# Kernel tuning notes

Hardware: AMD Instinct MI355X
Metric: run time of the kernel (lower is better)

## Reference

```python
import jax, jax.numpy as jnp
import numpy as np

B, L, H = 4, 2048, 1024
NH = 16
DK = H // NH


def setup_inputs() -> dict:
    key = jax.random.key(0)
    ks = jax.random.split(key, 9)
    s = 1.0 / np.sqrt(H)
    return {
        "x": jax.random.normal(ks[0], (B, L, H), dtype=jnp.float32),
        "Wq": jax.random.uniform(ks[1], (H, H), jnp.float32, -s, s),
        "bq": jnp.zeros((H,), jnp.float32),
        "Wk": jax.random.uniform(ks[2], (H, H), jnp.float32, -s, s),
        "bk": jnp.zeros((H,), jnp.float32),
        "Wv": jax.random.uniform(ks[3], (H, H), jnp.float32, -s, s),
        "bv": jnp.zeros((H,), jnp.float32),
        "Wo": jax.random.uniform(ks[4], (H, H), jnp.float32, -s, s),
        "bo": jnp.zeros((H,), jnp.float32),
    }


def reference(x, Wq, bq, Wk, bk, Wv, bv, Wo, bo):
    # Linear projections (torch Linear: x @ W.T + b), split heads -> (B, NH, L, DK)
    def proj(W, b):
        y = jnp.einsum("blh,oh->blo", x, W) + b
        return y.reshape(B, L, NH, DK).transpose(0, 2, 1, 3)

    q = proj(Wq, bq)
    k = proj(Wk, bk)
    v = proj(Wv, bv)

    scale = jnp.sqrt(jnp.asarray(DK, x.dtype))
    scores = jnp.einsum("bnqd,bnkd->bnqk", q, k) / scale  # (B, NH, L, L)
    attn = jax.nn.softmax(scores, axis=-1)
    # dropout is identity in eval mode
    context = jnp.einsum("bnqk,bnkd->bnqd", attn, v)
    context = context.transpose(0, 2, 1, 3).reshape(B, L, H)
    out = jnp.einsum("blh,oh->blo", context, Wo) + bo

    pooled = out.mean(axis=1)                 # (B, H)
    weights = attn.mean(axis=1).mean(axis=1)  # (B, L)
    return pooled, weights
```

## Files before the change

### kernel.cpp

```cpp
#include <hip/hip_runtime.h>
#include <math.h>

#define B_  4
#define L_  2048
#define H_  1024
#define NH_ 16
#define DK_ 64

#define QSC 0.18033688011112043f

typedef unsigned short ushort_t;
typedef __attribute__((ext_vector_type(8))) short short8;
typedef __attribute__((ext_vector_type(4))) float f32x4;

__device__ __forceinline__ ushort_t f2b(float f) {
    unsigned int u = __float_as_uint(f);
    return (ushort_t)((u + 0x7FFFu + ((u >> 16) & 1u)) >> 16);
}
__device__ __forceinline__ float b2f(ushort_t h) {
    return __uint_as_float(((unsigned int)h) << 16);
}
__device__ __forceinline__ float fexp2(float x) {
    return __builtin_amdgcn_exp2f(x);
}

__device__ __forceinline__ void gload_lds16(const void* g, void* l) {
    __builtin_amdgcn_global_load_lds((const __attribute__((address_space(1))) void*)g,
                                     (__attribute__((address_space(3))) void*)l, 16, 0, 0);
}

__device__ __forceinline__ void split8(const float4& a, const float4& b,
                                       short8& h, short8& l) {
    float f[8] = {a.x, a.y, a.z, a.w, b.x, b.y, b.z, b.w};
    #pragma unroll
    for (int e = 0; e < 8; ++e) {
        unsigned int u  = __float_as_uint(f[e]);
        float fh = __uint_as_float(u & 0xFFFF0000u);
        float r  = f[e] - fh;
        h[e] = (short)(u >> 16);
        l[e] = (short)(__float_as_uint(r) >> 16);
    }
}

__global__ __launch_bounds__(256) void wsplit_kernel(const float* __restrict__ src,
                                                     ushort_t* __restrict__ ph,
                                                     ushort_t* __restrict__ pl, int n4)
{
    int i = blockIdx.x * 256 + threadIdx.x;
    if (i < n4) {
        float4 v = ((const float4*)src)[i];
        ushort4 h, l;
        float f[4] = {v.x, v.y, v.z, v.w};
        ushort_t hh[4], ll[4];
        #pragma unroll
        for (int e = 0; e < 4; ++e) {
            hh[e] = f2b(f[e]);
            ll[e] = f2b(f[e] - b2f(hh[e]));
        }
        h.x = hh[0]; h.y = hh[1]; h.z = hh[2]; h.w = hh[3];
        l.x = ll[0]; l.y = ll[1]; l.z = ll[2]; l.w = ll[3];
        ((ushort4*)ph)[i] = h;
        ((ushort4*)pl)[i] = l;
    }
}

__global__ __launch_bounds__(256) void proj_split(
    const float* __restrict__ x,
    const ushort_t* __restrict__ Wqh, const ushort_t* __restrict__ Wql,
    const ushort_t* __restrict__ Wkh, const ushort_t* __restrict__ Wkl,
    const float* __restrict__ bq, const float* __restrict__ bk,
    ushort_t* __restrict__ qh, ushort_t* __restrict__ ql,
    ushort_t* __restrict__ kh, ushort_t* __restrict__ kl)
{
    const int z = blockIdx.z;
    const ushort_t* Wh = z ? Wkh : Wqh;
    const ushort_t* Wl = z ? Wkl : Wql;
    const float* bias  = z ? bk  : bq;
    ushort_t* dh       = z ? kh  : qh;
    ushort_t* dl       = z ? kl  : ql;
    const float qs     = z ? 1.0f : QSC;

    const int n0 = blockIdx.y * 128;
    const int o0 = blockIdx.x * 128;

    __shared__ float    Asf[128 * 32];
    __shared__ ushort_t Bsh[128 * 32];
    __shared__ ushort_t Bsl[128 * 32];

    const int t = threadIdx.x;
    const int lane = t & 63, w = t >> 6;
    const int ln = lane & 15, qd = lane >> 4;
    const int wy = w >> 1, wx = w & 1;

    int rxS[4], cxS[4];
    #pragma unroll
    for (int i = 0; i < 4; ++i) {
        int slot = i * 256 + t;
        rxS[i] = slot >> 3;
        cxS[i] = (slot & 7) ^ (rxS[i] & 7);
    }
    int rwS[2], cwS[2];
    #pragma unroll
    for (int i = 0; i < 2; ++i) {
        int slot = i * 256 + t;
        rwS[i] = slot >> 2;
        cwS[i] = (slot & 3) ^ ((rwS[i] >> 1) & 3);
    }

    f32x4 acc[4][4];
    #pragma unroll
    for (int i = 0; i < 4; ++i)
        #pragma unroll
        for (int j = 0; j < 4; ++j) acc[i][j] = (f32x4){0.f, 0.f, 0.f, 0.f};

    for (int k0 = 0; k0 < H_; k0 += 32) {
        __syncthreads();
        #pragma unroll
        for (int i = 0; i < 4; ++i)
            gload_lds16(x + (size_t)(n0 + rxS[i]) * H_ + k0 + cxS[i] * 4,
                        &Asf[i * 1024 + (t & ~63) * 4]);
        #pragma unroll
        for (int i = 0; i < 2; ++i) {
            gload_lds16(Wh + (size_t)(o0 + rwS[i]) * H_ + k0 + cwS[i] * 8,
                        &Bsh[i * 2048 + (t & ~63) * 8]);
            gload_lds16(Wl + (size_t)(o0 + rwS[i]) * H_ + k0 + cwS[i] * 8,
                        &Bsl[i * 2048 + (t & ~63) * 8]);
        }
        __syncthreads();

        short8 bh4[4], bl4[4];
        #pragma unroll
        for (int nt = 0; nt < 4; ++nt) {
            int row = wx * 64 + nt * 16 + ln;
            int sz = (qd ^ ((row >> 1) & 3)) << 3;
            bh4[nt] = *(const short8*)&Bsh[row * 32 + sz];
            bl4[nt] = *(const short8*)&Bsl[row * 32 + sz];
        }
        #pragma unroll
        for (int mt = 0; mt < 4; ++mt) {
            int row = wy * 64 + mt * 16 + ln;
            int r7 = row & 7;
            float4 fa = *(const float4*)&Asf[row * 32 + (((2 * qd)     ^ r7) << 2)];
            float4 fb = *(const float4*)&Asf[row * 32 + (((2 * qd + 1) ^ r7) << 2)];
            short8 ah, al;
            split8(fa, fb, ah, al);
            #pragma unroll
            for (int nt = 0; nt < 4; ++nt) {
                acc[mt][nt] = __builtin_amdgcn_mfma_f32_16x16x32_bf16(al, bh4[nt], acc[mt][nt], 0, 0, 0);
                acc[mt][nt] = __builtin_amdgcn_mfma_f32_16x16x32_bf16(ah, bl4[nt], acc[mt][nt], 0, 0, 0);
                acc[mt][nt] = __builtin_amdgcn_mfma_f32_16x16x32_bf16(ah, bh4[nt], acc[mt][nt], 0, 0, 0);
            }
        }
    }

    #pragma unroll
    for (int nt = 0; nt < 4; ++nt) {
        int o = o0 + wx * 64 + nt * 16 + ln;
        float bvv = bias[o];
        int hh = o >> 6, d = o & 63;
        #pragma unroll
        for (int mt = 0; mt < 4; ++mt) {
            #pragma unroll
            for (int r = 0; r < 4; ++r) {
                int n = n0 + wy * 64 + mt * 16 + qd * 4 + r;
                int bb = n >> 11, l = n & (L_ - 1);
                float val = (acc[mt][nt][r] + bvv) * qs;
                ushort_t vh = f2b(val);
                ushort_t vl = f2b(val - b2f(vh));
                size_t idx = (((size_t)(bb * NH_ + hh) * L_ + l) << 6) + d;
                dh[idx] = vh;
                dl[idx] = vl;
            }
        }
    }
}

__global__ __launch_bounds__(256) void attn_split(
    const ushort_t* __restrict__ qh, const ushort_t* __restrict__ ql,
    const ushort_t* __restrict__ kh, const ushort_t* __restrict__ kl,
    float* __restrict__ cs)
{
    const int qt = blockIdx.x & 15;
    const int bh = blockIdx.x >> 4;

    const int t = threadIdx.x;
    const int lane = t & 63, w = t >> 6;
    const int ln = lane & 15, qd = lane >> 4;

    __shared__ ushort_t Ksh[64 * 64];
    __shared__ ushort_t Ksl[64 * 64];
    __shared__ float cs_all[4][64];

    const size_t headoff = (size_t)bh * L_ * DK_;
    const size_t qoff0 = headoff + ((size_t)(qt * 128 + w * 32 + ln)) * DK_;
    const size_t qoff1 = qoff0 + 16 * DK_;
    short8 aqh[2][2], aql[2][2];
    aqh[0][0] = *(const short8*)(qh + qoff0 + qd * 8);
    aqh[0][1] = *(const short8*)(qh + qoff0 + 32 + qd * 8);
    aqh[1][0] = *(const short8*)(qh + qoff1 + qd * 8);
    aqh[1][1] = *(const short8*)(qh + qoff1 + 32 + qd * 8);
    aql[0][0] = *(const short8*)(ql + qoff0 + qd * 8);
    aql[0][1] = *(const short8*)(ql + qoff0 + 32 + qd * 8);
    aql[1][0] = *(const short8*)(ql + qoff1 + qd * 8);
    aql[1][1] = *(const short8*)(ql + qoff1 + 32 + qd * 8);

    int rowS[2], cS[2];
    #pragma unroll
    for (int i = 0; i < 2; ++i) {
        int slot = i * 256 + t;
        rowS[i] = slot >> 3;
        cS[i] = (slot & 7) ^ (rowS[i] & 7);
    }

    float l_run[2][4] = {};

    for (int kt = 0; kt < 32; ++kt) {
        __syncthreads();
        #pragma unroll
        for (int i = 0; i < 2; ++i)
            gload_lds16(kh + headoff + ((size_t)(kt * 64 + rowS[i]) << 6) + cS[i] * 8,
                        &Ksh[i * 2048 + (t & ~63) * 8]);
        __syncthreads();

        #pragma unroll
        for (int nt = 0; nt < 4; ++nt) {
            int kr = nt * 16 + ln;
            int sz0 = ((qd     ^ (kr & 7)) << 3);
            int sz1 = (((qd + 4) ^ (kr & 7)) << 3);
            short8 b0h = *(const short8*)&Ksh[kr * 64 + sz0];
            short8 b1h = *(const short8*)&Ksh[kr * 64 + sz1];
            #pragma unroll
            for (int s = 0; s < 2; ++s) {
                f32x4 zz = (f32x4){0.f, 0.f, 0.f, 0.f};
                zz = __builtin_amdgcn_mfma_f32_16x16x32_bf16(aqh[s][0], b0h, zz, 0, 0, 0);
                zz = __builtin_amdgcn_mfma_f32_16x16x32_bf16(aqh[s][1], b1h, zz, 0, 0, 0);
                #pragma unroll
                for (int r = 0; r < 4; ++r)
                    l_run[s][r] += fexp2(zz[r]);
            }
        }
    }

    #pragma unroll
    for (int off = 1; off < 16; off <<= 1)
        #pragma unroll
        for (int s = 0; s < 2; ++s)
            #pragma unroll
            for (int r = 0; r < 4; ++r)
                l_run[s][r] += __shfl_xor(l_run[s][r], off);
    float inv_l[2][4];
    #pragma unroll
    for (int s = 0; s < 2; ++s)
        #pragma unroll
        for (int r = 0; r < 4; ++r) inv_l[s][r] = 1.0f / l_run[s][r];

    for (int kt = 0; kt < 32; ++kt) {
        __syncthreads();
        #pragma unroll
        for (int i = 0; i < 2; ++i) {
            gload_lds16(kh + headoff + ((size_t)(kt * 64 + rowS[i]) << 6) + cS[i] * 8,
                        &Ksh[i * 2048 + (t & ~63) * 8]);
            gload_lds16(kl + headoff + ((size_t)(kt * 64 + rowS[i]) << 6) + cS[i] * 8,
                        &Ksl[i * 2048 + (t & ~63) * 8]);
        }
        __syncthreads();

        float colp[4];
        #pragma unroll
        for (int nt = 0; nt < 4; ++nt) {
            int kr = nt * 16 + ln;
            int sz0 = ((qd     ^ (kr & 7)) << 3);
            int sz1 = (((qd + 4) ^ (kr & 7)) << 3);
            short8 b0h = *(const short8*)&Ksh[kr * 64 + sz0];
            short8 b1h = *(const short8*)&Ksh[kr * 64 + sz1];
            short8 b0l = *(const short8*)&Ksl[kr * 64 + sz0];
            short8 b1l = *(const short8*)&Ksl[kr * 64 + sz1];
            float cp = 0.f;
            #pragma unroll
            for (int s = 0; s < 2; ++s) {
                f32x4 zz = (f32x4){0.f, 0.f, 0.f, 0.f};
                zz = __builtin_amdgcn_mfma_f32_16x16x32_bf16(aql[s][0], b0h, zz, 0, 0, 0);
                zz = __builtin_amdgcn_mfma_f32_16x16x32_bf16(aql[s][1], b1h, zz, 0, 0, 0);
                zz = __builtin_amdgcn_mfma_f32_16x16x32_bf16(aqh[s][0], b0l, zz, 0, 0, 0);
                zz = __builtin_amdgcn_mfma_f32_16x16x32_bf16(aqh[s][1], b1l, zz, 0, 0, 0);
                zz = __builtin_amdgcn_mfma_f32_16x16x32_bf16(aqh[s][0], b0h, zz, 0, 0, 0);
                zz = __builtin_amdgcn_mfma_f32_16x16x32_bf16(aqh[s][1], b1h, zz, 0, 0, 0);
                cp += fexp2(zz[0]) * inv_l[s][0] + fexp2(zz[1]) * inv_l[s][1]
                    + fexp2(zz[2]) * inv_l[s][2] + fexp2(zz[3]) * inv_l[s][3];
            }
            colp[nt] = cp;
        }
        #pragma unroll
        for (int nt = 0; nt < 4; ++nt) {
            colp[nt] += __shfl_xor(colp[nt], 16);
            colp[nt] += __shfl_xor(colp[nt], 32);
        }
        float mine = (qd == 0) ? colp[0] : (qd == 1) ? colp[1] : (qd == 2) ? colp[2] : colp[3];
        cs_all[w][lane] = mine;
        __syncthreads();
        if (t < 64) {
            float tot = cs_all[0][t] + cs_all[1][t] + cs_all[2][t] + cs_all[3][t];
            atomicAdd(&cs[(size_t)bh * L_ + kt * 64 + t], tot);
        }
    }
}

__global__ __launch_bounds__(256) void ctx1_kernel(
    const float* __restrict__ cs, const float* __restrict__ x, float* __restrict__ T)
{
    const int o0 = blockIdx.x * 64, b = blockIdx.y, l0 = blockIdx.z * 256;
    const int t = threadIdx.x, o = t & 63, hg = t >> 6;
    __shared__ float cs_s[16][128];
    float acc[4] = {};

    for (int ch = 0; ch < 2; ++ch) {
        int lbase = l0 + ch * 128;
        __syncthreads();
        for (int i = t; i < 2048; i += 256) {
            int h = i >> 7, lc = i & 127;
            cs_s[h][lc] = cs[((size_t)(b * NH_ + h) << 11) + lbase + lc];
        }
        __syncthreads();
        for (int lc = 0; lc < 128; ++lc) {
            float xv = x[((size_t)(b * L_ + lbase + lc) << 10) + o0 + o];
            #pragma unroll
            for (int j = 0; j < 4; ++j) acc[j] += cs_s[hg * 4 + j][lc] * xv;
        }
    }
    #pragma unroll
    for (int j = 0; j < 4; ++j)
        atomicAdd(&T[((size_t)(b * NH_ + hg * 4 + j) << 10) + o0 + o], acc[j]);
}

__global__ __launch_bounds__(256) void ctx2_kernel(
    const float* __restrict__ T, const float* __restrict__ Wv,
    const float* __restrict__ bv, float* __restrict__ ctx)
{
    const int gid  = blockIdx.x * 4 + (threadIdx.x >> 6);
    const int lane = threadIdx.x & 63;
    const int b = gid >> 10, o = gid & (H_ - 1);
    const float4* wr = (const float4*)(Wv + (size_t)o * H_);
    const float4* tr = (const float4*)(T + ((size_t)(b * NH_ + (o >> 6)) << 10));
    float acc = 0.f;
    #pragma unroll
    for (int i = 0; i < 4; ++i) {
        float4 wv = wr[lane + i * 64];
        float4 tv = tr[lane + i * 64];
        acc += wv.x * tv.x + wv.y * tv.y + wv.z * tv.z + wv.w * tv.w;
    }
    #pragma unroll
    for (int off = 32; off; off >>= 1) acc += __shfl_xor(acc, off);
    if (lane == 0) ctx[(b << 10) + o] = acc + (float)L_ * bv[o];
}

__global__ __launch_bounds__(256) void pooled_kernel(
    const float* __restrict__ ctx, const float* __restrict__ Wo,
    const float* __restrict__ bo, float* __restrict__ out)
{
    const int gid  = blockIdx.x * 4 + (threadIdx.x >> 6);
    const int lane = threadIdx.x & 63;
    const int b = gid >> 10, o = gid & (H_ - 1);
    const float4* wr = (const float4*)(Wo + (size_t)o * H_);
    const float4* cr = (const float4*)(ctx + ((size_t)b << 10));
    float acc = 0.f;
    #pragma unroll
    for (int i = 0; i < 4; ++i) {
        float4 wv = wr[lane + i * 64];
        float4 cv = cr[lane + i * 64];
        acc += wv.x * cv.x + wv.y * cv.y + wv.z * cv.z + wv.w * cv.w;
    }
    #pragma unroll
    for (int off = 32; off; off >>= 1) acc += __shfl_xor(acc, off);
    if (lane == 0) out[(b << 10) + o] = acc * (1.0f / (float)L_) + bo[o];
}

__global__ void weights_kernel(const float* __restrict__ cs, float* __restrict__ out)
{
    int i = blockIdx.x * 256 + threadIdx.x;
    int b = i >> 11, k = i & (L_ - 1);
    float s = 0.f;
    #pragma unroll
    for (int h = 0; h < NH_; ++h) s += cs[((size_t)(b * NH_ + h) << 11) + k];
    out[B_ * H_ + i] = s * (1.0f / (float)(NH_ * L_));
}

extern "C" void kernel_launch(void* const* d_in, const int* in_sizes, int n_in,
                              void* d_out, int out_size, void* d_ws, size_t ws_size,
                              hipStream_t stream)
{
    const float* x  = (const float*)d_in[0];
    const float* Wq = (const float*)d_in[1];
    const float* bq = (const float*)d_in[2];
    const float* Wk = (const float*)d_in[3];
    const float* bk = (const float*)d_in[4];
    const float* Wv = (const float*)d_in[5];
    const float* bv = (const float*)d_in[6];
    const float* Wo = (const float*)d_in[7];
    const float* bo = (const float*)d_in[8];
    float* out = (float*)d_out;

    float* ws  = (float*)d_ws;
    float* cs  = ws;
    float* T   = ws + 131072;
    float* ctx = ws + 196608;
    ushort_t* base = (ushort_t*)(ws + 200704);
    const size_t QE = 8388608;
    ushort_t* qhb = base;
    ushort_t* qlb = base + QE;
    ushort_t* khb = base + 2 * QE;
    ushort_t* klb = base + 3 * QE;
    ushort_t* wqh = base + 4 * QE;
    ushort_t* wql = wqh + 1048576;
    ushort_t* wkh = wql + 1048576;
    ushort_t* wkl = wkh + 1048576;

    hipMemsetAsync(ws, 0, (131072 + 65536) * sizeof(float), stream);

    wsplit_kernel<<<1024, 256, 0, stream>>>(Wq, wqh, wql, 262144);
    wsplit_kernel<<<1024, 256, 0, stream>>>(Wk, wkh, wkl, 262144);

    proj_split<<<dim3(8, 64, 2), 256, 0, stream>>>(x, wqh, wql, wkh, wkl, bq, bk,
                                                   qhb, qlb, khb, klb);

    attn_split<<<B_ * NH_ * (L_ / 128), 256, 0, stream>>>(qhb, qlb, khb, klb, cs);

    ctx1_kernel<<<dim3(16, 4, 8), 256, 0, stream>>>(cs, x, T);
    ctx2_kernel<<<1024, 256, 0, stream>>>(T, Wv, bv, ctx);
    pooled_kernel<<<1024, 256, 0, stream>>>(ctx, Wo, bo, out);
    weights_kernel<<<(B_ * L_) / 256, 256, 0, stream>>>(cs, out);
}
```

Before: 386.0 us.

## Drop Q low-part terms and presplit x into bf16 hi/lo

Q is now stored only as a rounded bf16 high part, so the attention score computation drops two of its six MFMAs per tile and the Q projection drops the Wq-low term and the Q-low output. The activations x are split into bf16 hi/lo once by a separate kernel instead of being split in every projection tile, which removes repeated per-tile conversion work. This lowers attention compute and memory traffic but reduces precision of the Q·K scores, and it adds an extra pass over x plus its write.

```diff
diff --git a/kernel.cpp b/kernel.cpp
--- a/kernel.cpp
+++ b/kernel.cpp
@@ -29,20 +29,7 @@
                                      (__attribute__((address_space(3))) void*)l, 16, 0, 0);
 }
 
-__device__ __forceinline__ void split8(const float4& a, const float4& b,
-                                       short8& h, short8& l) {
-    float f[8] = {a.x, a.y, a.z, a.w, b.x, b.y, b.z, b.w};
-    #pragma unroll
-    for (int e = 0; e < 8; ++e) {
-        unsigned int u  = __float_as_uint(f[e]);
-        float fh = __uint_as_float(u & 0xFFFF0000u);
-        float r  = f[e] - fh;
-        h[e] = (short)(u >> 16);
-        l[e] = (short)(__float_as_uint(r) >> 16);
-    }
-}
-
-__global__ __launch_bounds__(256) void wsplit_kernel(const float* __restrict__ src,
+__global__ __launch_bounds__(256) void fsplit_kernel(const float* __restrict__ src,
                                                      ushort_t* __restrict__ ph,
                                                      ushort_t* __restrict__ pl, int n4)
 {
@@ -65,25 +52,23 @@
 }
 
 __global__ __launch_bounds__(256) void proj_split(
-    const float* __restrict__ x,
-    const ushort_t* __restrict__ Wqh, const ushort_t* __restrict__ Wql,
+    const ushort_t* __restrict__ xh, const ushort_t* __restrict__ xl,
+    const ushort_t* __restrict__ Wqh,
     const ushort_t* __restrict__ Wkh, const ushort_t* __restrict__ Wkl,
     const float* __restrict__ bq, const float* __restrict__ bk,
-    ushort_t* __restrict__ qh, ushort_t* __restrict__ ql,
-    ushort_t* __restrict__ kh, ushort_t* __restrict__ kl)
+    ushort_t* __restrict__ qho,
+    ushort_t* __restrict__ kho, ushort_t* __restrict__ klo)
 {
     const int z = blockIdx.z;
     const ushort_t* Wh = z ? Wkh : Wqh;
-    const ushort_t* Wl = z ? Wkl : Wql;
+    const ushort_t* Wl = Wkl;
     const float* bias  = z ? bk  : bq;
-    ushort_t* dh       = z ? kh  : qh;
-    ushort_t* dl       = z ? kl  : ql;
-    const float qs     = z ? 1.0f : QSC;
 
     const int n0 = blockIdx.y * 128;
     const int o0 = blockIdx.x * 128;
 
-    __shared__ float    Asf[128 * 32];
+    __shared__ ushort_t Ash[128 * 32];
+    __shared__ ushort_t Asl[128 * 32];
     __shared__ ushort_t Bsh[128 * 32];
     __shared__ ushort_t Bsl[128 * 32];
 
@@ -91,20 +76,14 @@
     const int lane = t & 63, w = t >> 6;
     const int ln = lane & 15, qd = lane >> 4;
     const int wy = w >> 1, wx = w & 1;
-
-    int rxS[4], cxS[4];
-    #pragma unroll
-    for (int i = 0; i < 4; ++i) {
-        int slot = i * 256 + t;
-        rxS[i] = slot >> 3;
-        cxS[i] = (slot & 7) ^ (rxS[i] & 7);
-    }
-    int rwS[2], cwS[2];
+    const int ldsbase = (t & ~63) * 8;
+
+    int rowS[2], cS[2];
     #pragma unroll
     for (int i = 0; i < 2; ++i) {
         int slot = i * 256 + t;
-        rwS[i] = slot >> 2;
-        cwS[i] = (slot & 3) ^ ((rwS[i] >> 1) & 3);
+        rowS[i] = slot >> 2;
+        cS[i] = (slot & 3) ^ ((rowS[i] >> 1) & 3);
     }
 
     f32x4 acc[4][4];
@@ -116,15 +95,19 @@
     for (int k0 = 0; k0 < H_; k0 += 32) {
         __syncthreads();
         #pragma unroll
-        for (int i = 0; i < 4; ++i)
-            gload_lds16(x + (size_t)(n0 + rxS[i]) * H_ + k0 + cxS[i] * 4,
-                        &Asf[i * 1024 + (t & ~63) * 4]);
-        #pragma unroll
         for (int i = 0; i < 2; ++i) {
-            gload_lds16(Wh + (size_t)(o0 + rwS[i]) * H_ + k0 + cwS[i] * 8,
-                        &Bsh[i * 2048 + (t & ~63) * 8]);
-            gload_lds16(Wl + (size_t)(o0 + rwS[i]) * H_ + k0 + cwS[i] * 8,
-                        &Bsl[i * 2048 + (t & ~63) * 8]);
+            gload_lds16(xh + (size_t)(n0 + rowS[i]) * H_ + k0 + cS[i] * 8,
+                        &Ash[i * 2048 + ldsbase]);
+            gload_lds16(xl + (size_t)(n0 + rowS[i]) * H_ + k0 + cS[i] * 8,
+                        &Asl[i * 2048 + ldsbase]);
+            gload_lds16(Wh + (size_t)(o0 + rowS[i]) * H_ + k0 + cS[i] * 8,
+                        &Bsh[i * 2048 + ldsbase]);
+        }
+        if (z) {
+            #pragma unroll
+            for (int i = 0; i < 2; ++i)
+                gload_lds16(Wl + (size_t)(o0 + rowS[i]) * H_ + k0 + cS[i] * 8,
+                            &Bsl[i * 2048 + ldsbase]);
         }
         __syncthreads();
 
@@ -134,21 +117,27 @@
             int row = wx * 64 + nt * 16 + ln;
             int sz = (qd ^ ((row >> 1) & 3)) << 3;
             bh4[nt] = *(const short8*)&Bsh[row * 32 + sz];
-            bl4[nt] = *(const short8*)&Bsl[row * 32 + sz];
+            if (z) bl4[nt] = *(const short8*)&Bsl[row * 32 + sz];
         }
         #pragma unroll
         for (int mt = 0; mt < 4; ++mt) {
             int row = wy * 64 + mt * 16 + ln;
-            int r7 = row & 7;
-            float4 fa = *(const float4*)&Asf[row * 32 + (((2 * qd)     ^ r7) << 2)];
-            float4 fb = *(const float4*)&Asf[row * 32 + (((2 * qd + 1) ^ r7) << 2)];
-            short8 ah, al;
-            split8(fa, fb, ah, al);
-            #pragma unroll
-            for (int nt = 0; nt < 4; ++nt) {
-                acc[mt][nt] = __builtin_amdgcn_mfma_f32_16x16x32_bf16(al, bh4[nt], acc[mt][nt], 0, 0, 0);
-                acc[mt][nt] = __builtin_amdgcn_mfma_f32_16x16x32_bf16(ah, bl4[nt], acc[mt][nt], 0, 0, 0);
-                acc[mt][nt] = __builtin_amdgcn_mfma_f32_16x16x32_bf16(ah, bh4[nt], acc[mt][nt], 0, 0, 0);
+            int sz = (qd ^ ((row >> 1) & 3)) << 3;
+            short8 ah = *(const short8*)&Ash[row * 32 + sz];
+            short8 al = *(const short8*)&Asl[row * 32 + sz];
+            if (z) {
+                #pragma unroll
+                for (int nt = 0; nt < 4; ++nt) {
+                    acc[mt][nt] = __builtin_amdgcn_mfma_f32_16x16x32_bf16(al, bh4[nt], acc[mt][nt], 0, 0, 0);
+                    acc[mt][nt] = __builtin_amdgcn_mfma_f32_16x16x32_bf16(ah, bl4[nt], acc[mt][nt], 0, 0, 0);
+                    acc[mt][nt] = __builtin_amdgcn_mfma_f32_16x16x32_bf16(ah, bh4[nt], acc[mt][nt], 0, 0, 0);
+                }
+            } else {
+                #pragma unroll
+                for (int nt = 0; nt < 4; ++nt) {
+                    acc[mt][nt] = __builtin_amdgcn_mfma_f32_16x16x32_bf16(al, bh4[nt], acc[mt][nt], 0, 0, 0);
+                    acc[mt][nt] = __builtin_amdgcn_mfma_f32_16x16x32_bf16(ah, bh4[nt], acc[mt][nt], 0, 0, 0);
+                }
             }
         }
     }
@@ -164,19 +153,22 @@
             for (int r = 0; r < 4; ++r) {
                 int n = n0 + wy * 64 + mt * 16 + qd * 4 + r;
                 int bb = n >> 11, l = n & (L_ - 1);
-                float val = (acc[mt][nt][r] + bvv) * qs;
-                ushort_t vh = f2b(val);
-                ushort_t vl = f2b(val - b2f(vh));
                 size_t idx = (((size_t)(bb * NH_ + hh) * L_ + l) << 6) + d;
-                dh[idx] = vh;
-                dl[idx] = vl;
+                float val = acc[mt][nt][r] + bvv;
+                if (z) {
+                    ushort_t vh = f2b(val);
+                    kho[idx] = vh;
+                    klo[idx] = f2b(val - b2f(vh));
+                } else {
+                    qho[idx] = f2b(val * QSC);
+                }
             }
         }
     }
 }
 
 __global__ __launch_bounds__(256) void attn_split(
-    const ushort_t* __restrict__ qh, const ushort_t* __restrict__ ql,
+    const ushort_t* __restrict__ qh,
     const ushort_t* __restrict__ kh, const ushort_t* __restrict__ kl,
     float* __restrict__ cs)
 {
@@ -194,15 +186,11 @@
     const size_t headoff = (size_t)bh * L_ * DK_;
     const size_t qoff0 = headoff + ((size_t)(qt * 128 + w * 32 + ln)) * DK_;
     const size_t qoff1 = qoff0 + 16 * DK_;
-    short8 aqh[2][2], aql[2][2];
+    short8 aqh[2][2];
     aqh[0][0] = *(const short8*)(qh + qoff0 + qd * 8);
     aqh[0][1] = *(const short8*)(qh + qoff0 + 32 + qd * 8);
     aqh[1][0] = *(const short8*)(qh + qoff1 + qd * 8);
     aqh[1][1] = *(const short8*)(qh + qoff1 + 32 + qd * 8);
-    aql[0][0] = *(const short8*)(ql + qoff0 + qd * 8);
-    aql[0][1] = *(const short8*)(ql + qoff0 + 32 + qd * 8);
-    aql[1][0] = *(const short8*)(ql + qoff1 + qd * 8);
-    aql[1][1] = *(const short8*)(ql + qoff1 + 32 + qd * 8);
 
     int rowS[2], cS[2];
     #pragma unroll
@@ -279,8 +267,6 @@
             #pragma unroll
             for (int s = 0; s < 2; ++s) {
                 f32x4 zz = (f32x4){0.f, 0.f, 0.f, 0.f};
-                zz = __builtin_amdgcn_mfma_f32_16x16x32_bf16(aql[s][0], b0h, zz, 0, 0, 0);
-                zz = __builtin_amdgcn_mfma_f32_16x16x32_bf16(aql[s][1], b1h, zz, 0, 0, 0);
                 zz = __builtin_amdgcn_mfma_f32_16x16x32_bf16(aqh[s][0], b0l, zz, 0, 0, 0);
                 zz = __builtin_amdgcn_mfma_f32_16x16x32_bf16(aqh[s][1], b1l, zz, 0, 0, 0);
                 zz = __builtin_amdgcn_mfma_f32_16x16x32_bf16(aqh[s][0], b0h, zz, 0, 0, 0);
@@ -406,23 +392,25 @@
     ushort_t* base = (ushort_t*)(ws + 200704);
     const size_t QE = 8388608;
     ushort_t* qhb = base;
-    ushort_t* qlb = base + QE;
-    ushort_t* khb = base + 2 * QE;
-    ushort_t* klb = base + 3 * QE;
-    ushort_t* wqh = base + 4 * QE;
+    ushort_t* khb = base + QE;
+    ushort_t* klb = base + 2 * QE;
+    ushort_t* xhb = base + 3 * QE;
+    ushort_t* xlb = base + 4 * QE;
+    ushort_t* wqh = base + 5 * QE;
     ushort_t* wql = wqh + 1048576;
     ushort_t* wkh = wql + 1048576;
     ushort_t* wkl = wkh + 1048576;
 
     hipMemsetAsync(ws, 0, (131072 + 65536) * sizeof(float), stream);
 
-    wsplit_kernel<<<1024, 256, 0, stream>>>(Wq, wqh, wql, 262144);
-    wsplit_kernel<<<1024, 256, 0, stream>>>(Wk, wkh, wkl, 262144);
-
-    proj_split<<<dim3(8, 64, 2), 256, 0, stream>>>(x, wqh, wql, wkh, wkl, bq, bk,
-                                                   qhb, qlb, khb, klb);
-
-    attn_split<<<B_ * NH_ * (L_ / 128), 256, 0, stream>>>(qhb, qlb, khb, klb, cs);
+    fsplit_kernel<<<8192, 256, 0, stream>>>(x,  xhb, xlb, 2097152);
+    fsplit_kernel<<<1024, 256, 0, stream>>>(Wq, wqh, wql, 262144);
+    fsplit_kernel<<<1024, 256, 0, stream>>>(Wk, wkh, wkl, 262144);
+
+    proj_split<<<dim3(8, 64, 2), 256, 0, stream>>>(xhb, xlb, wqh, wkh, wkl,
+                                                   bq, bk, qhb, khb, klb);
+
+    attn_split<<<B_ * NH_ * (L_ / 128), 256, 0, stream>>>(qhb, khb, klb, cs);
 
     ctx1_kernel<<<dim3(16, 4, 8), 256, 0, stream>>>(cs, x, T);
     ctx2_kernel<<<1024, 256, 0, stream>>>(T, Wv, bv, ctx);
```

Result: faster. 366.0 us (-5.2%).
